# Kernel tuning notes

Hardware: AMD Instinct MI355X
Metric: run time of the kernel (lower is better)

The kernel has to match this reference:

```python
import jax, jax.numpy as jnp
import numpy as np

N = 100000   # nodes
E = 3200000  # edges (avg degree 32)
H = 75       # hidden
ITER = 3     # num_layers


def setup_inputs() -> dict:
    key = jax.random.key(0)
    ks = jax.random.split(key, 16)
    s = 0.1  # weight scale
    x = jax.random.normal(ks[0], (N, H), jnp.float32)
    src = jax.random.randint(ks[1], (E,), 0, N)
    dst = jax.random.randint(ks[2], (E,), 0, N)
    edge_index = jnp.stack([src, dst]).astype(jnp.int32)
    rn = lambda k, shp: jax.random.normal(k, shp, jnp.float32) * s
    return {
        "x": x,
        "edge_index": edge_index,
        "eps": jnp.zeros((1,), jnp.float32),      # GIN train_eps, init 0
        "w1": rn(ks[3], (H, H)), "b1": jnp.zeros((H,), jnp.float32),
        "w2": rn(ks[4], (H, H)), "b2": jnp.zeros((H,), jnp.float32),
        "w_ih": rn(ks[5], (3 * H, H)), "w_hh": rn(ks[6], (3 * H, H)),
        "b_ih": jnp.zeros((3 * H,), jnp.float32), "b_hh": jnp.zeros((3 * H,), jnp.float32),
        "wc1": rn(ks[7], (ITER * H, 2 * H)), "bc1": jnp.zeros((2 * H,), jnp.float32),
        "wc2": rn(ks[8], (2 * H, H)), "bc2": jnp.zeros((H,), jnp.float32),
    }


def reference(x, edge_index, eps, w1, b1, w2, b2, w_ih, w_hh, b_ih, b_hh, wc1, bc1, wc2, bc2):
    src, dst = edge_index[0], edge_index[1]

    def gin(xt):
        # sum aggregation over incoming edges (gather -> scatter-add)
        agg = jax.ops.segment_sum(xt[src], dst, num_segments=N)
        z = (1.0 + eps[0]) * xt + agg
        return jnp.maximum(z @ w1 + b1, 0.0) @ w2 + b2

    def gru_step(inp, h):
        # torch.nn.GRU single step; gate order: r, z, n
        gi = inp @ w_ih.T + b_ih
        gh = h @ w_hh.T + b_hh
        ir, iz, inn = jnp.split(gi, 3, axis=-1)
        hr, hz, hn = jnp.split(gh, 3, axis=-1)
        r = jax.nn.sigmoid(ir + hr)
        zg = jax.nn.sigmoid(iz + hz)
        n = jnp.tanh(inn + r * hn)
        return (1.0 - zg) * n + zg * h

    h = x   # h0 = x.unsqueeze(0)
    xt = x
    node_states = []
    for _ in range(ITER):
        m = jnp.maximum(gin(xt), 0.0)
        h = gru_step(m, h)
        xt = h  # GRU output == hidden state for single layer/step
        node_states.append(xt)

    cat = jnp.concatenate(node_states, axis=1)  # [N, ITER*H]
    readout = jnp.maximum(cat @ wc1 + bc1, 0.0) @ wc2 + bc2
    return (xt, readout)
```

## Files before the change

### kernel.cpp

```cpp
#include <hip/hip_runtime.h>

#define NN 100000
#define EE 3200000
#define N2 100032
#define NBUCK 782
#define CPAD 16
#define CHUNK 12288
#define CAP 5120

typedef _Float16 f16;
typedef _Float16 f16x8 __attribute__((ext_vector_type(8)));
typedef float f32x4 __attribute__((ext_vector_type(4)));
typedef unsigned int u32;

#define MFMA(a, b, c) __builtin_amdgcn_mfma_f32_16x16x32_f16((a), (b), (c), 0, 0, 0)


__global__ __launch_bounds__(256) void initcur_kernel(int* __restrict__ bcur) {
  int i = blockIdx.x * 256 + threadIdx.x;
  if (i < NBUCK) bcur[i * CPAD] = i * CAP;
}

__global__ __launch_bounds__(256) void binB_kernel(const int* __restrict__ src,
                                                   const int* __restrict__ dst,
                                                   int* __restrict__ bcur,
                                                   u32* __restrict__ ebuf) {
  __shared__ int hist[NBUCK];
  __shared__ int base[NBUCK];
  int tid = threadIdx.x;
  int e0 = blockIdx.x * CHUNK;
  int e1 = e0 + CHUNK;
  if (e1 > EE) e1 = EE;
  for (int i = tid; i < NBUCK; i += 256) hist[i] = 0;
  __syncthreads();
  for (int e = e0 + tid * 4; e < e1; e += 1024) {
    int4 d = *(const int4*)(dst + e);
    atomicAdd(&hist[d.x >> 7], 1);
    atomicAdd(&hist[d.y >> 7], 1);
    atomicAdd(&hist[d.z >> 7], 1);
    atomicAdd(&hist[d.w >> 7], 1);
  }
  __syncthreads();
  for (int i = tid; i < NBUCK; i += 256) {
    int c = hist[i];
    if (c) base[i] = atomicAdd(&bcur[i * CPAD], c);
  }
  __syncthreads();
  for (int i = tid; i < NBUCK; i += 256) hist[i] = 0;
  __syncthreads();
  for (int e = e0 + tid * 4; e < e1; e += 1024) {
    int4 d = *(const int4*)(dst + e);
    int4 s = *(const int4*)(src + e);
    int b, loc;
    b = d.x >> 7; loc = atomicAdd(&hist[b], 1);
    ebuf[base[b] + loc] = (u32)s.x | ((u32)(d.x & 127) << 17);
    b = d.y >> 7; loc = atomicAdd(&hist[b], 1);
    ebuf[base[b] + loc] = (u32)s.y | ((u32)(d.y & 127) << 17);
    b = d.z >> 7; loc = atomicAdd(&hist[b], 1);
    ebuf[base[b] + loc] = (u32)s.z | ((u32)(d.z & 127) << 17);
    b = d.w >> 7; loc = atomicAdd(&hist[b], 1);
    ebuf[base[b] + loc] = (u32)s.w | ((u32)(d.w & 127) << 17);
  }
}

__global__ __launch_bounds__(256) void binC_kernel(const u32* __restrict__ ebuf,
                                                   const int* __restrict__ bcur,
                                                   int* __restrict__ st,
                                                   int* __restrict__ ct,
                                                   int* __restrict__ csr) {
  __shared__ int cnt[128], sc[128], cur[128];
  int b = blockIdx.x, tid = threadIdx.x;
  int e0 = b * CAP;
  int e1 = bcur[b * CPAD];
  if (tid < 128) cnt[tid] = 0;
  __syncthreads();
  for (int e = e0 + tid; e < e1; e += 256) atomicAdd(&cnt[ebuf[e] >> 17], 1);
  __syncthreads();
  if (tid < 128) sc[tid] = cnt[tid];
  __syncthreads();
  for (int off = 1; off < 128; off <<= 1) {
    int t = 0;
    if (tid < 128 && tid >= off) t = sc[tid - off];
    __syncthreads();
    if (tid < 128) sc[tid] += t;
    __syncthreads();
  }
  if (tid < 128) {
    int gpos = e0 + sc[tid] - cnt[tid];
    int node = b * 128 + tid;
    if (node < NN) {
      st[node] = gpos;
      ct[node] = cnt[tid];
    }
    cur[tid] = gpos;
  }
  __syncthreads();
  for (int e = e0 + tid; e < e1; e += 256) {
    u32 p = ebuf[e];
    int pos = atomicAdd(&cur[p >> 17], 1);
    csr[pos] = (int)(p & 0x1FFFFu);
  }
}


__device__ __forceinline__ f16 pack_one(const float* __restrict__ W,
                                        const float* __restrict__ bias, int rel, int K, int Nc,
                                        int KG, int trans, int bslot) {
  int e = rel & 7, nn = (rel >> 3) & 15;
  int g = (rel >> 7) % KG, nb = (rel >> 7) / KG;
  int k = g * 8 + e, n = nb * 16 + nn;
  float v = 0.f;
  if (n < Nc) {
    if (k < K) v = trans ? W[n * K + k] : W[k * Nc + n];
    else if (k == bslot) v = bias[n];
  }
  return (f16)v;
}

__global__ __launch_bounds__(256) void prep_kernel(const float* __restrict__ x,
                                                   f16* __restrict__ xp,
                                                   f16* __restrict__ xc,
                                                   f16* __restrict__ zm,
                                                   const float* __restrict__ w1,
                                                   const float* __restrict__ b1,
                                                   const float* __restrict__ w2,
                                                   const float* __restrict__ b2,
                                                   const float* __restrict__ wih,
                                                   const float* __restrict__ bih,
                                                   const float* __restrict__ whh,
                                                   const float* __restrict__ bhh,
                                                   const float* __restrict__ wc1,
                                                   const float* __restrict__ bc1,
                                                   const float* __restrict__ wc2,
                                                   const float* __restrict__ bc2,
                                                   f16* __restrict__ wp) {
  int b = blockIdx.x, tid = threadIdx.x;
  if (b < 470) {
    int i = b * 256 + tid;
    if (i >= 120320) return;
    f16 v;
    if (i < 7680) v = pack_one(w1, b1, i, 75, 75, 12, 0, 95);
    else if (i < 15360) v = pack_one(w2, b2, i - 7680, 75, 75, 12, 0, 95);
    else if (i < 38400) {
      int r = i - 15360, g = r / 7680;
      v = pack_one(wih + g * 5625, bih + g * 75, r - g * 7680, 75, 75, 12, 1, 95);
    } else if (i < 61440) {
      int r = i - 38400, g = r / 7680;
      v = pack_one(whh + g * 5625, bhh + g * 75, r - g * 7680, 75, 75, 12, 1, 95);
    } else if (i < 107520) {
      int rel = i - 61440;
      int e = rel & 7, nn = (rel >> 3) & 15;
      int g = (rel >> 7) % 36, nb = (rel >> 7) / 36;
      int q = g * 8 + e, buf = q / 96, kk = q - buf * 96, n = nb * 16 + nn;
      float f = 0.f;
      if (n < 150) {
        if (kk < 75) f = wc1[(buf * 75 + kk) * 150 + n];
        else if (kk == 95 && buf == 0) f = bc1[n];
      }
      v = (f16)f;
    } else v = pack_one(wc2, bc2, i - 107520, 150, 75, 20, 0, 159);
    wp[i] = v;
  } else if (b < 6722) {
    int i = (b - 470) * 256 + tid;
    int r = i >> 4, c = i & 15;
    zm[r * 96 + 80 + c] = (f16)(c == 15 ? 1.f : 0.f);
  } else if (b < 44234) {
    int i = (b - 6722) * 256 + tid;
    int r = i / 96, c = i - r * 96;
    float v = (r < NN && c < 75) ? x[r * 75 + c] : (c == 95 ? 1.f : 0.f);
    xp[i] = (f16)v;
  } else {
    int i = (b - 44234) * 256 + tid;
    int r = i / 80, c = i - r * 80;
    float v = (r < NN && c < 75) ? x[r * 75 + c] : 0.f;
    xc[i] = (f16)v;
  }
}


__global__ __launch_bounds__(256) void aggz_kernel(const f16* __restrict__ xc,
                                                   const int* __restrict__ st,
                                                   const int* __restrict__ ct,
                                                   const int* __restrict__ csr,
                                                   const float* __restrict__ eps,
                                                   f16* __restrict__ zm) {
  int tid = threadIdx.x;
  int l = tid & 63;
  int n = blockIdx.x * 4 + (tid >> 6);
  if (n >= NN) return;
  int s = l / 10, j = l - s * 10;
  int e0 = st[n], e1 = e0 + ct[n];
  float acc[8] = {0, 0, 0, 0, 0, 0, 0, 0};
  if (l < 60) {
#pragma unroll 4
    for (int e = e0 + s; e < e1; e += 6) {
      int sr = csr[e];
      f16x8 v = *(const f16x8*)(xc + sr * 80 + j * 8);
#pragma unroll
      for (int k = 0; k < 8; ++k) acc[k] += (float)v[k];
    }
  }
  int l1 = (l + 30) & 63, l2 = (l + 10) & 63, l3 = (l + 20) & 63;
#pragma unroll
  for (int k = 0; k < 8; ++k) {
    float t = __shfl(acc[k], l1, 64);
    if (l < 30) acc[k] += t;
    t = __shfl(acc[k], l2, 64);
    if (l < 10) acc[k] += t;
    t = __shfl(acc[k], l3, 64);
    if (l < 10) acc[k] += t;
  }
  if (l < 10) {
    f16x8 self = *(const f16x8*)(xc + n * 80 + j * 8);
    float ep = 1.f + eps[0];
    f16x8 o;
#pragma unroll
    for (int k = 0; k < 8; ++k) o[k] = (f16)(ep * (float)self[k] + acc[k]);
    *(f16x8*)(zm + n * 96 + j * 8) = o;
  }
}


__global__ __launch_bounds__(256) void mlpgru_kernel(const f16* __restrict__ zm,
                                                     const f16* __restrict__ hcur,
                                                     const f16* __restrict__ w1p,
                                                     const f16* __restrict__ w2p,
                                                     const f16* __restrict__ wihp,
                                                     const f16* __restrict__ whhp,
                                                     f16* __restrict__ hb_out,
                                                     f16* __restrict__ hc_out,
                                                     float* __restrict__ outx) {
  __shared__ f16 Ls[4][16 * 104];
  __shared__ f16 Hs[4][16 * 104];
  int tid = threadIdx.x;
  int w = tid >> 6, l = tid & 63, lm = l & 15, lg = l >> 4;
  int row0 = blockIdx.x * 64 + w * 16;
  const f16* ar = zm + (row0 + lm) * 96;
  const f16* hr = hcur + (row0 + lm) * 96;
  f16x8 a0 = *(const f16x8*)(ar + lg * 8);
  f16x8 a1 = *(const f16x8*)(ar + 32 + lg * 8);
  f16x8 a2 = *(const f16x8*)(ar + 64 + lg * 8);
  f16x8 h0 = *(const f16x8*)(hr + lg * 8);
  f16x8 h1 = *(const f16x8*)(hr + 32 + lg * 8);
  f16x8 h2 = *(const f16x8*)(hr + 64 + lg * 8);
  f16* Hd = Hs[w];
  *(f16x8*)(Hd + lm * 104 + lg * 8) = h0;
  *(f16x8*)(Hd + lm * 104 + 32 + lg * 8) = h1;
  *(f16x8*)(Hd + lm * 104 + 64 + lg * 8) = h2;
  f16* Ld = Ls[w];
#pragma unroll
  for (int nb = 0; nb < 5; ++nb) {
    const f16* bp = w1p + ((nb * 12 + lg) * 16 + lm) * 8;
    f32x4 acc = (f32x4){0.f, 0.f, 0.f, 0.f};
    acc = MFMA(a0, *(const f16x8*)bp, acc);
    acc = MFMA(a1, *(const f16x8*)(bp + 512), acc);
    acc = MFMA(a2, *(const f16x8*)(bp + 1024), acc);
#pragma unroll
    for (int r = 0; r < 4; ++r)
      Ld[(lg * 4 + r) * 104 + nb * 16 + lm] = (f16)fmaxf(acc[r], 0.f);
  }
#pragma unroll
  for (int c = 0; c < 4; ++c) {
    int col = 80 + lg * 4 + c;
    Ld[lm * 104 + col] = (f16)(col == 95 ? 1.f : 0.f);
  }
  const f16* Lr = Ld + lm * 104;
  f16x8 c0 = *(const f16x8*)(Lr + lg * 8);
  f16x8 c1 = *(const f16x8*)(Lr + 32 + lg * 8);
  f16x8 c2 = *(const f16x8*)(Lr + 64 + lg * 8);
#pragma unroll
  for (int nb = 0; nb < 5; ++nb) {
    const f16* bp = w2p + ((nb * 12 + lg) * 16 + lm) * 8;
    f32x4 acc = (f32x4){0.f, 0.f, 0.f, 0.f};
    acc = MFMA(c0, *(const f16x8*)bp, acc);
    acc = MFMA(c1, *(const f16x8*)(bp + 512), acc);
    acc = MFMA(c2, *(const f16x8*)(bp + 1024), acc);
#pragma unroll
    for (int r = 0; r < 4; ++r)
      Ld[(lg * 4 + r) * 104 + nb * 16 + lm] = (f16)fmaxf(acc[r], 0.f);
  }
  f16x8 am0 = *(const f16x8*)(Lr + lg * 8);
  f16x8 am1 = *(const f16x8*)(Lr + 32 + lg * 8);
  f16x8 am2 = *(const f16x8*)(Lr + 64 + lg * 8);
#pragma unroll 1
  for (int nb = 0; nb < 5; ++nb) {
    f32x4 rg = (f32x4){0.f, 0.f, 0.f, 0.f};
    f32x4 zg = rg, ni = rg, nh = rg;
#pragma unroll
    for (int s = 0; s < 3; ++s) {
      f16x8 ams = (s == 0) ? am0 : (s == 1) ? am1 : am2;
      f16x8 ahs = (s == 0) ? h0 : (s == 1) ? h1 : h2;
      int fo = ((nb * 12 + s * 4 + lg) * 16 + lm) * 8;
      rg = MFMA(ams, *(const f16x8*)(wihp + fo), rg);
      rg = MFMA(ahs, *(const f16x8*)(whhp + fo), rg);
      zg = MFMA(ams, *(const f16x8*)(wihp + 7680 + fo), zg);
      zg = MFMA(ahs, *(const f16x8*)(whhp + 7680 + fo), zg);
      ni = MFMA(ams, *(const f16x8*)(wihp + 15360 + fo), ni);
      nh = MFMA(ahs, *(const f16x8*)(whhp + 15360 + fo), nh);
    }
#pragma unroll
    for (int r = 0; r < 4; ++r) {
      int n = nb * 16 + lm;
      float hval = (float)Hd[(lg * 4 + r) * 104 + n];
      float rv = 1.f / (1.f + __expf(-rg[r]));
      float zv = 1.f / (1.f + __expf(-zg[r]));
      float u = ni[r] + rv * nh[r];
      float t = __expf(-2.f * fabsf(u));
      float nv = copysignf((1.f - t) / (1.f + t), u);
      float hp = zv * (hval - nv) + nv;
      Ld[(lg * 4 + r) * 104 + n] = (f16)hp;
    }
  }
#pragma unroll
  for (int k = 0; k < 3; ++k) {
    int p = l + 64 * k;
    int r = p / 12, sl = p - r * 12;
    f16x8 v = *(const f16x8*)(Ld + r * 104 + sl * 8);
    *(f16x8*)(hb_out + (row0 + r) * 96 + sl * 8) = v;
  }
  if (hc_out) {
#pragma unroll
    for (int k = 0; k < 3; ++k) {
      int p = l + 64 * k;
      if (p < 160) {
        int r = p / 10, sl = p - r * 10;
        f16x8 v = *(const f16x8*)(Ld + r * 104 + sl * 8);
        *(f16x8*)(hc_out + (row0 + r) * 80 + sl * 8) = v;
      }
    }
  }
  if (outx) {
    for (int k = 0; k < 19; ++k) {
      int p = l + 64 * k;
      int gi = row0 * 75 + p;
      if (p < 1200 && gi < NN * 75) {
        int r = p / 75, c = p - r * 75;
        outx[gi] = (float)Ld[r * 104 + c];
      }
    }
  }
}


__global__ __launch_bounds__(256) void readout_kernel(const f16* __restrict__ hb0,
                                                      const f16* __restrict__ hb1,
                                                      const f16* __restrict__ hb2,
                                                      const f16* __restrict__ wc1p,
                                                      const f16* __restrict__ wc2p,
                                                      float* __restrict__ out) {
  __shared__ f16 Ls[4][16 * 168];
  int tid = threadIdx.x;
  int w = tid >> 6, l = tid & 63, lm = l & 15, lg = l >> 4;
  int row0 = blockIdx.x * 64 + w * 16;
  int row = row0 + lm;
  f16x8 a[9];
#pragma unroll
  for (int s = 0; s < 9; ++s) {
    const f16* hb = (s < 3) ? hb0 : (s < 6) ? hb1 : hb2;
    a[s] = *(const f16x8*)(hb + row * 96 + (4 * (s - (s / 3) * 3) + lg) * 8);
  }
  f16* Ld = Ls[w];
#pragma unroll
  for (int nb = 0; nb < 10; ++nb) {
    f32x4 acc = (f32x4){0.f, 0.f, 0.f, 0.f};
#pragma unroll
    for (int s = 0; s < 9; ++s)
      acc = MFMA(a[s], *(const f16x8*)(wc1p + ((nb * 36 + 4 * s + lg) * 16 + lm) * 8), acc);
#pragma unroll
    for (int r = 0; r < 4; ++r) {
      int n = nb * 16 + lm;
      float v = fmaxf(acc[r], 0.f);
      if (n >= 150) v = (n == 159) ? 1.f : 0.f;
      Ld[(lg * 4 + r) * 168 + n] = (f16)v;
    }
  }
  const f16* Lr = Ls[w] + lm * 168;
  f16x8 a2[5];
#pragma unroll
  for (int s = 0; s < 5; ++s) a2[s] = *(const f16x8*)(Lr + s * 32 + lg * 8);
  f32x4 acc2[5];
#pragma unroll
  for (int nb = 0; nb < 5; ++nb) {
    acc2[nb] = (f32x4){0.f, 0.f, 0.f, 0.f};
#pragma unroll
    for (int s = 0; s < 5; ++s)
      acc2[nb] = MFMA(a2[s], *(const f16x8*)(wc2p + ((nb * 20 + s * 4 + lg) * 16 + lm) * 8),
                      acc2[nb]);
  }
  float* Lf = (float*)Ls[w];
#pragma unroll
  for (int nb = 0; nb < 5; ++nb)
#pragma unroll
    for (int r = 0; r < 4; ++r) {
      int n = nb * 16 + lm;
      if (n < 75) Lf[(lg * 4 + r) * 76 + n] = acc2[nb][r];
    }
  for (int k = 0; k < 19; ++k) {
    int p = l + 64 * k;
    int gi = row0 * 75 + p;
    if (p < 1200 && gi < NN * 75) {
      int r = p / 75, c = p - r * 75;
      out[gi] = Lf[r * 76 + c];
    }
  }
}


extern "C" void kernel_launch(void* const* d_in, const int* in_sizes, int n_in,
                              void* d_out, int out_size, void* d_ws, size_t ws_size,
                              hipStream_t stream) {
  const float* x    = (const float*)d_in[0];
  const int*   ei   = (const int*)d_in[1];
  const float* eps  = (const float*)d_in[2];
  const float* w1   = (const float*)d_in[3];
  const float* b1   = (const float*)d_in[4];
  const float* w2   = (const float*)d_in[5];
  const float* b2   = (const float*)d_in[6];
  const float* w_ih = (const float*)d_in[7];
  const float* w_hh = (const float*)d_in[8];
  const float* b_ih = (const float*)d_in[9];
  const float* b_hh = (const float*)d_in[10];
  const float* wc1  = (const float*)d_in[11];
  const float* bc1  = (const float*)d_in[12];
  const float* wc2  = (const float*)d_in[13];
  const float* bc2  = (const float*)d_in[14];

  const int* srcv = ei;
  const int* dstv = ei + EE;

  float* out_x = (float*)d_out;
  float* out_r = out_x + NN * 75;

  f16* zm   = (f16*)d_ws;
  f16* x0   = zm + (size_t)N2 * 96;
  f16* hb0  = x0 + (size_t)N2 * 96;
  f16* hb1  = hb0 + (size_t)N2 * 96;
  f16* hb2  = hb1 + (size_t)N2 * 96;
  f16* hc   = hb2 + (size_t)N2 * 96;
  f16* wp   = hc + (size_t)N2 * 80;
  f16* w1p  = wp;
  f16* w2p  = wp + 7680;
  f16* wihp = wp + 15360;
  f16* whhp = wp + 38400;
  f16* wc1p = wp + 61440;
  f16* wc2p = wp + 107520;
  u32* ebuf = (u32*)(wp + 120320);
  int* csr  = (int*)(ebuf + (size_t)NBUCK * CAP);
  int* st   = csr + (size_t)NBUCK * CAP;
  int* ctv  = st + NN;
  int* bcur = ctv + NN;

  initcur_kernel<<<4, 256, 0, stream>>>(bcur);
  binB_kernel<<<(EE + CHUNK - 1) / CHUNK, 256, 0, stream>>>(srcv, dstv, bcur, ebuf);
  binC_kernel<<<NBUCK, 256, 0, stream>>>(ebuf, bcur, st, ctv, csr);
  prep_kernel<<<75494, 256, 0, stream>>>(x, x0, hc, zm, w1, b1, w2, b2, w_ih, b_ih,
                                         w_hh, b_hh, wc1, bc1, wc2, bc2, wp);

  int gb = N2 / 64;
  f16* hbs[3] = {hb0, hb1, hb2};
  for (int it = 0; it < 3; ++it) {
    const f16* h = (it == 0) ? x0 : hbs[it - 1];
    aggz_kernel<<<25000, 256, 0, stream>>>(hc, st, ctv, csr, eps, zm);
    mlpgru_kernel<<<gb, 256, 0, stream>>>(zm, h, w1p, w2p, wihp, whhp, hbs[it],
                                          (it < 2) ? hc : nullptr,
                                          (it == 2) ? out_x : nullptr);
  }
  readout_kernel<<<gb, 256, 0, stream>>>(hb0, hb1, hb2, wc1p, wc2p, out_r);
}
```

Before: 557.1 us.

## Fuse edge binning with prep, drop compact feature copy, memset bucket cursors

New measurement: 548.0 us. No clear change (-1.6%).

```diff
diff --git a/kernel.cpp b/kernel.cpp
--- a/kernel.cpp
+++ b/kernel.cpp
@@ -7,6 +7,7 @@
 #define CPAD 16
 #define CHUNK 12288
 #define CAP 5120
+#define NB_BINB 261
 
 typedef _Float16 f16;
 typedef _Float16 f16x8 __attribute__((ext_vector_type(8)));
@@ -14,93 +15,6 @@
 typedef unsigned int u32;
 
 #define MFMA(a, b, c) __builtin_amdgcn_mfma_f32_16x16x32_f16((a), (b), (c), 0, 0, 0)
-
-
-__global__ __launch_bounds__(256) void initcur_kernel(int* __restrict__ bcur) {
-  int i = blockIdx.x * 256 + threadIdx.x;
-  if (i < NBUCK) bcur[i * CPAD] = i * CAP;
-}
-
-__global__ __launch_bounds__(256) void binB_kernel(const int* __restrict__ src,
-                                                   const int* __restrict__ dst,
-                                                   int* __restrict__ bcur,
-                                                   u32* __restrict__ ebuf) {
-  __shared__ int hist[NBUCK];
-  __shared__ int base[NBUCK];
-  int tid = threadIdx.x;
-  int e0 = blockIdx.x * CHUNK;
-  int e1 = e0 + CHUNK;
-  if (e1 > EE) e1 = EE;
-  for (int i = tid; i < NBUCK; i += 256) hist[i] = 0;
-  __syncthreads();
-  for (int e = e0 + tid * 4; e < e1; e += 1024) {
-    int4 d = *(const int4*)(dst + e);
-    atomicAdd(&hist[d.x >> 7], 1);
-    atomicAdd(&hist[d.y >> 7], 1);
-    atomicAdd(&hist[d.z >> 7], 1);
-    atomicAdd(&hist[d.w >> 7], 1);
-  }
-  __syncthreads();
-  for (int i = tid; i < NBUCK; i += 256) {
-    int c = hist[i];
-    if (c) base[i] = atomicAdd(&bcur[i * CPAD], c);
-  }
-  __syncthreads();
-  for (int i = tid; i < NBUCK; i += 256) hist[i] = 0;
-  __syncthreads();
-  for (int e = e0 + tid * 4; e < e1; e += 1024) {
-    int4 d = *(const int4*)(dst + e);
-    int4 s = *(const int4*)(src + e);
-    int b, loc;
-    b = d.x >> 7; loc = atomicAdd(&hist[b], 1);
-    ebuf[base[b] + loc] = (u32)s.x | ((u32)(d.x & 127) << 17);
-    b = d.y >> 7; loc = atomicAdd(&hist[b], 1);
-    ebuf[base[b] + loc] = (u32)s.y | ((u32)(d.y & 127) << 17);
-    b = d.z >> 7; loc = atomicAdd(&hist[b], 1);
-    ebuf[base[b] + loc] = (u32)s.z | ((u32)(d.z & 127) << 17);
-    b = d.w >> 7; loc = atomicAdd(&hist[b], 1);
-    ebuf[base[b] + loc] = (u32)s.w | ((u32)(d.w & 127) << 17);
-  }
-}
-
-__global__ __launch_bounds__(256) void binC_kernel(const u32* __restrict__ ebuf,
-                                                   const int* __restrict__ bcur,
-                                                   int* __restrict__ st,
-                                                   int* __restrict__ ct,
-                                                   int* __restrict__ csr) {
-  __shared__ int cnt[128], sc[128], cur[128];
-  int b = blockIdx.x, tid = threadIdx.x;
-  int e0 = b * CAP;
-  int e1 = bcur[b * CPAD];
-  if (tid < 128) cnt[tid] = 0;
-  __syncthreads();
-  for (int e = e0 + tid; e < e1; e += 256) atomicAdd(&cnt[ebuf[e] >> 17], 1);
-  __syncthreads();
-  if (tid < 128) sc[tid] = cnt[tid];
-  __syncthreads();
-  for (int off = 1; off < 128; off <<= 1) {
-    int t = 0;
-    if (tid < 128 && tid >= off) t = sc[tid - off];
-    __syncthreads();
-    if (tid < 128) sc[tid] += t;
-    __syncthreads();
-  }
-  if (tid < 128) {
-    int gpos = e0 + sc[tid] - cnt[tid];
-    int node = b * 128 + tid;
-    if (node < NN) {
-      st[node] = gpos;
-      ct[node] = cnt[tid];
-    }
-    cur[tid] = gpos;
-  }
-  __syncthreads();
-  for (int e = e0 + tid; e < e1; e += 256) {
-    u32 p = ebuf[e];
-    int pos = atomicAdd(&cur[p >> 17], 1);
-    csr[pos] = (int)(p & 0x1FFFFu);
-  }
-}
 
 
 __device__ __forceinline__ f16 pack_one(const float* __restrict__ W,
@@ -117,26 +31,66 @@
   return (f16)v;
 }
 
-__global__ __launch_bounds__(256) void prep_kernel(const float* __restrict__ x,
-                                                   f16* __restrict__ xp,
-                                                   f16* __restrict__ xc,
-                                                   f16* __restrict__ zm,
-                                                   const float* __restrict__ w1,
-                                                   const float* __restrict__ b1,
-                                                   const float* __restrict__ w2,
-                                                   const float* __restrict__ b2,
-                                                   const float* __restrict__ wih,
-                                                   const float* __restrict__ bih,
-                                                   const float* __restrict__ whh,
-                                                   const float* __restrict__ bhh,
-                                                   const float* __restrict__ wc1,
-                                                   const float* __restrict__ bc1,
-                                                   const float* __restrict__ wc2,
-                                                   const float* __restrict__ bc2,
-                                                   f16* __restrict__ wp) {
+
+__global__ __launch_bounds__(256) void binBprep_kernel(const int* __restrict__ src,
+                                                       const int* __restrict__ dst,
+                                                       int* __restrict__ bcur,
+                                                       u32* __restrict__ ebuf,
+                                                       const float* __restrict__ x,
+                                                       f16* __restrict__ xp,
+                                                       f16* __restrict__ zm,
+                                                       const float* __restrict__ w1,
+                                                       const float* __restrict__ b1,
+                                                       const float* __restrict__ w2,
+                                                       const float* __restrict__ b2,
+                                                       const float* __restrict__ wih,
+                                                       const float* __restrict__ bih,
+                                                       const float* __restrict__ whh,
+                                                       const float* __restrict__ bhh,
+                                                       const float* __restrict__ wc1,
+                                                       const float* __restrict__ bc1,
+                                                       const float* __restrict__ wc2,
+                                                       const float* __restrict__ bc2,
+                                                       f16* __restrict__ wp) {
+  __shared__ int hist[NBUCK];
+  __shared__ int base[NBUCK];
   int b = blockIdx.x, tid = threadIdx.x;
-  if (b < 470) {
-    int i = b * 256 + tid;
+  if (b < NB_BINB) {
+    int e0 = b * CHUNK;
+    int e1 = e0 + CHUNK;
+    if (e1 > EE) e1 = EE;
+    for (int i = tid; i < NBUCK; i += 256) hist[i] = 0;
+    __syncthreads();
+    for (int e = e0 + tid * 4; e < e1; e += 1024) {
+      int4 d = *(const int4*)(dst + e);
+      atomicAdd(&hist[d.x >> 7], 1);
+      atomicAdd(&hist[d.y >> 7], 1);
+      atomicAdd(&hist[d.z >> 7], 1);
+      atomicAdd(&hist[d.w >> 7], 1);
+    }
+    __syncthreads();
+    for (int i = tid; i < NBUCK; i += 256) {
+      int c = hist[i];
+      if (c) base[i] = i * CAP + atomicAdd(&bcur[i * CPAD], c);
+    }
+    __syncthreads();
+    for (int i = tid; i < NBUCK; i += 256) hist[i] = 0;
+    __syncthreads();
+    for (int e = e0 + tid * 4; e < e1; e += 1024) {
+      int4 d = *(const int4*)(dst + e);
+      int4 s = *(const int4*)(src + e);
+      int bb, loc;
+      bb = d.x >> 7; loc = atomicAdd(&hist[bb], 1);
+      ebuf[base[bb] + loc] = (u32)s.x | ((u32)(d.x & 127) << 17);
+      bb = d.y >> 7; loc = atomicAdd(&hist[bb], 1);
+      ebuf[base[bb] + loc] = (u32)s.y | ((u32)(d.y & 127) << 17);
+      bb = d.z >> 7; loc = atomicAdd(&hist[bb], 1);
+      ebuf[base[bb] + loc] = (u32)s.z | ((u32)(d.z & 127) << 17);
+      bb = d.w >> 7; loc = atomicAdd(&hist[bb], 1);
+      ebuf[base[bb] + loc] = (u32)s.w | ((u32)(d.w & 127) << 17);
+    }
+  } else if (b < NB_BINB + 470) {
+    int i = (b - NB_BINB) * 256 + tid;
     if (i >= 120320) return;
     f16 v;
     if (i < 7680) v = pack_one(w1, b1, i, 75, 75, 12, 0, 95);
@@ -160,20 +114,55 @@
       v = (f16)f;
     } else v = pack_one(wc2, bc2, i - 107520, 150, 75, 20, 0, 159);
     wp[i] = v;
-  } else if (b < 6722) {
-    int i = (b - 470) * 256 + tid;
+  } else if (b < NB_BINB + 470 + 6252) {
+    int i = (b - NB_BINB - 470) * 256 + tid;
     int r = i >> 4, c = i & 15;
     zm[r * 96 + 80 + c] = (f16)(c == 15 ? 1.f : 0.f);
-  } else if (b < 44234) {
-    int i = (b - 6722) * 256 + tid;
+  } else {
+    int i = (b - NB_BINB - 470 - 6252) * 256 + tid;
     int r = i / 96, c = i - r * 96;
     float v = (r < NN && c < 75) ? x[r * 75 + c] : (c == 95 ? 1.f : 0.f);
     xp[i] = (f16)v;
-  } else {
-    int i = (b - 44234) * 256 + tid;
-    int r = i / 80, c = i - r * 80;
-    float v = (r < NN && c < 75) ? x[r * 75 + c] : 0.f;
-    xc[i] = (f16)v;
+  }
+}
+
+
+__global__ __launch_bounds__(256) void binC_kernel(const u32* __restrict__ ebuf,
+                                                   const int* __restrict__ bcur,
+                                                   int* __restrict__ st,
+                                                   int* __restrict__ ct,
+                                                   int* __restrict__ csr) {
+  __shared__ int cnt[128], sc[128], cur[128];
+  int b = blockIdx.x, tid = threadIdx.x;
+  int e0 = b * CAP;
+  int e1 = e0 + bcur[b * CPAD];
+  if (tid < 128) cnt[tid] = 0;
+  __syncthreads();
+  for (int e = e0 + tid; e < e1; e += 256) atomicAdd(&cnt[ebuf[e] >> 17], 1);
+  __syncthreads();
+  if (tid < 128) sc[tid] = cnt[tid];
+  __syncthreads();
+  for (int off = 1; off < 128; off <<= 1) {
+    int t = 0;
+    if (tid < 128 && tid >= off) t = sc[tid - off];
+    __syncthreads();
+    if (tid < 128) sc[tid] += t;
+    __syncthreads();
+  }
+  if (tid < 128) {
+    int gpos = e0 + sc[tid] - cnt[tid];
+    int node = b * 128 + tid;
+    if (node < NN) {
+      st[node] = gpos;
+      ct[node] = cnt[tid];
+    }
+    cur[tid] = gpos;
+  }
+  __syncthreads();
+  for (int e = e0 + tid; e < e1; e += 256) {
+    u32 p = ebuf[e];
+    int pos = atomicAdd(&cur[p >> 17], 1);
+    csr[pos] = (int)(p & 0x1FFFFu);
   }
 }
 
@@ -195,7 +184,7 @@
 #pragma unroll 4
     for (int e = e0 + s; e < e1; e += 6) {
       int sr = csr[e];
-      f16x8 v = *(const f16x8*)(xc + sr * 80 + j * 8);
+      f16x8 v = *(const f16x8*)(xc + sr * 96 + j * 8);
 #pragma unroll
       for (int k = 0; k < 8; ++k) acc[k] += (float)v[k];
     }
@@ -211,7 +200,7 @@
     if (l < 10) acc[k] += t;
   }
   if (l < 10) {
-    f16x8 self = *(const f16x8*)(xc + n * 80 + j * 8);
+    f16x8 self = *(const f16x8*)(xc + n * 96 + j * 8);
     float ep = 1.f + eps[0];
     f16x8 o;
 #pragma unroll
@@ -228,7 +217,6 @@
                                                      const f16* __restrict__ wihp,
                                                      const f16* __restrict__ whhp,
                                                      f16* __restrict__ hb_out,
-                                                     f16* __restrict__ hc_out,
                                                      float* __restrict__ outx) {
   __shared__ f16 Ls[4][16 * 104];
   __shared__ f16 Hs[4][16 * 104];
@@ -318,17 +306,6 @@
     f16x8 v = *(const f16x8*)(Ld + r * 104 + sl * 8);
     *(f16x8*)(hb_out + (row0 + r) * 96 + sl * 8) = v;
   }
-  if (hc_out) {
-#pragma unroll
-    for (int k = 0; k < 3; ++k) {
-      int p = l + 64 * k;
-      if (p < 160) {
-        int r = p / 10, sl = p - r * 10;
-        f16x8 v = *(const f16x8*)(Ld + r * 104 + sl * 8);
-        *(f16x8*)(hc_out + (row0 + r) * 80 + sl * 8) = v;
-      }
-    }
-  }
   if (outx) {
     for (int k = 0; k < 19; ++k) {
       int p = l + 64 * k;
@@ -436,8 +413,7 @@
   f16* hb0  = x0 + (size_t)N2 * 96;
   f16* hb1  = hb0 + (size_t)N2 * 96;
   f16* hb2  = hb1 + (size_t)N2 * 96;
-  f16* hc   = hb2 + (size_t)N2 * 96;
-  f16* wp   = hc + (size_t)N2 * 80;
+  f16* wp   = hb2 + (size_t)N2 * 96;
   f16* w1p  = wp;
   f16* w2p  = wp + 7680;
   f16* wihp = wp + 15360;
@@ -450,19 +426,18 @@
   int* ctv  = st + NN;
   int* bcur = ctv + NN;
 
-  initcur_kernel<<<4, 256, 0, stream>>>(bcur);
-  binB_kernel<<<(EE + CHUNK - 1) / CHUNK, 256, 0, stream>>>(srcv, dstv, bcur, ebuf);
+  hipMemsetAsync(bcur, 0, NBUCK * CPAD * sizeof(int), stream);
+  binBprep_kernel<<<44495, 256, 0, stream>>>(srcv, dstv, bcur, ebuf,
+                                             x, x0, zm, w1, b1, w2, b2, w_ih, b_ih,
+                                             w_hh, b_hh, wc1, bc1, wc2, bc2, wp);
   binC_kernel<<<NBUCK, 256, 0, stream>>>(ebuf, bcur, st, ctv, csr);
-  prep_kernel<<<75494, 256, 0, stream>>>(x, x0, hc, zm, w1, b1, w2, b2, w_ih, b_ih,
-                                         w_hh, b_hh, wc1, bc1, wc2, bc2, wp);
 
   int gb = N2 / 64;
   f16* hbs[3] = {hb0, hb1, hb2};
   for (int it = 0; it < 3; ++it) {
     const f16* h = (it == 0) ? x0 : hbs[it - 1];
-    aggz_kernel<<<25000, 256, 0, stream>>>(hc, st, ctv, csr, eps, zm);
+    aggz_kernel<<<25000, 256, 0, stream>>>(h, st, ctv, csr, eps, zm);
     mlpgru_kernel<<<gb, 256, 0, stream>>>(zm, h, w1p, w2p, wihp, whhp, hbs[it],
-                                          (it < 2) ? hc : nullptr,
                                           (it == 2) ? out_x : nullptr);
   }
   readout_kernel<<<gb, 256, 0, stream>>>(hb0, hb1, hb2, wc1p, wc2p, out_r);
```
